# Kernel optimization log

Hardware: AMD Instinct MI355X
Metric: run time of the kernel (lower is better)

## Reference

```python
import jax, jax.numpy as jnp
import numpy as np

B, L, E, H, W = 2, 8192, 1024, 16, 128
HD = E // H  # 64


def setup_inputs() -> dict:
    key = jax.random.key(0)
    ks = jax.random.split(key, 9)
    s = 1.0 / np.sqrt(E)
    inp = {"x": jax.random.normal(ks[0], (B, L, E), jnp.float32)}
    for i, n in enumerate(["Wq", "Wk", "Wv", "Wo"]):
        inp[n] = jax.random.uniform(ks[1 + i], (E, E), jnp.float32, -s, s)
    for i, n in enumerate(["bq", "bk", "bv", "bo"]):
        inp[n] = jax.random.uniform(ks[5 + i], (E,), jnp.float32, -s, s)
    return inp


def _skew_prob(p, w):
    # (..., w, 2w+1) -> (..., w, 3w) with row i right-shifted by i:
    # out[..., i, i+j] = p[..., i, j]  (zeros elsewhere)
    lead = p.shape[:-2]
    M, Lc = p.shape[-2], p.shape[-1]
    p = jnp.pad(p, [(0, 0)] * len(lead) + [(0, 0), (0, M + 1)])
    p = p.reshape(*lead, M * (Lc + M + 1))[..., :-M].reshape(*lead, M, M + Lc)
    return p[..., :-1]


def _sliding_attend(q, k, v, w):
    # q,k,v: (b,h,l,d); banded attention, window w on each side (2w+1 diagonals)
    b, h, l, d = q.shape
    c = l // w
    qc = q.reshape(b, h, c, w, d)
    # per-chunk key/value windows of 3w tokens (w halo each side, zero padded)
    idx = jnp.arange(c)[:, None] * w + jnp.arange(3 * w)[None, :]  # (c, 3w)
    kw = jnp.pad(k, ((0, 0), (0, 0), (w, w), (0, 0)))[:, :, idx]  # (b,h,c,3w,d)
    s = jnp.einsum('bhcqd,bhckd->bhcqk', qc, kw)  # (b,h,c,w,3w)
    # extract band: band[i, j] = s[i, i+j], j in [0, 2w] (offset d = j - w)
    gidx = (jnp.arange(w)[:, None] + jnp.arange(2 * w + 1)[None, :])[None, None, None]
    band = jnp.take_along_axis(s, gidx, axis=-1).reshape(b, h, l, 2 * w + 1)
    # mask out-of-range positions (matches the module's edge -inf loop)
    pos = jnp.arange(l)[:, None] + (jnp.arange(2 * w + 1) - w)[None, :]
    band = jnp.where((pos >= 0) & (pos < l), band, -jnp.inf)
    prob = jax.nn.softmax(band / np.sqrt(d), axis=-1)  # scale by sqrt(head_dim)
    vw = jnp.pad(v, ((0, 0), (0, 0), (w, w), (0, 0)))[:, :, idx]  # (b,h,c,3w,d)
    p3 = _skew_prob(prob.reshape(b, h, c, w, 2 * w + 1), w)  # (b,h,c,w,3w)
    ctx = jnp.einsum('bhcqk,bhckd->bhcqd', p3, vw)
    return ctx.reshape(b, h, l, d)


def reference(x, Wq, Wk, Wv, Wo, bq, bk, bv, bo):
    q = (x @ Wq.T + bq).reshape(B, L, H, HD).transpose(0, 2, 1, 3)
    k = (x @ Wk.T + bk).reshape(B, L, H, HD).transpose(0, 2, 1, 3)
    v = (x @ Wv.T + bv).reshape(B, L, H, HD).transpose(0, 2, 1, 3)
    ctx = _sliding_attend(q, k, v, W)
    ctx = ctx.transpose(0, 2, 1, 3).reshape(B, L, E)
    return ctx @ Wo.T + bo
```

## Files before the change

### kernel.cpp

```cpp
#include <hip/hip_runtime.h>
#include <math.h>

#define B_SZ  2
#define L_SEQ 8192
#define EMB   1024
#define NH    16
#define HDIM  64
#define WIN   128
#define MROWS (B_SZ*L_SEQ)

typedef __attribute__((ext_vector_type(8))) _Float16 f16x8;
typedef __attribute__((ext_vector_type(4))) _Float16 f16x4;
typedef __attribute__((ext_vector_type(4))) float f32x4;

__device__ __forceinline__ void gload16(const void* g, void* l) {
    __builtin_amdgcn_global_load_lds(
        (const __attribute__((address_space(1))) unsigned int*)g,
        (__attribute__((address_space(3))) unsigned int*)l, 16, 0, 0);
}

__global__ __launch_bounds__(256)
void round_all(const float* __restrict__ x,
               const float* __restrict__ wq, const float* __restrict__ wk,
               const float* __restrict__ wv, const float* __restrict__ wo,
               _Float16* __restrict__ xf, _Float16* __restrict__ q16,
               _Float16* __restrict__ k16, _Float16* __restrict__ v16,
               _Float16* __restrict__ o16)
{
    const size_t NX = (size_t)MROWS * EMB, NW = (size_t)EMB * EMB;
    size_t gid = ((size_t)blockIdx.x * 256 + threadIdx.x) * 4;
    const float* src; _Float16* dst; size_t off;
    if (gid < NX)               { src = x;  dst = xf;  off = gid; }
    else if (gid < NX + NW)     { src = wq; dst = q16; off = gid - NX; }
    else if (gid < NX + 2*NW)   { src = wk; dst = k16; off = gid - NX - 2*NW + NW; }
    else if (gid < NX + 3*NW)   { src = wv; dst = v16; off = gid - NX - 2*NW; }
    else                        { src = wo; dst = o16; off = gid - NX - 3*NW; }
    float4 v = *(const float4*)(src + off);
    f16x4 o;
    o[0] = (_Float16)v.x; o[1] = (_Float16)v.y;
    o[2] = (_Float16)v.z; o[3] = (_Float16)v.w;
    *(f16x4*)(dst + off) = o;
}


#define GEMM_CORE(Aptr, Bptr)                                                  \
    const int t = threadIdx.x;                                                 \
    const int wave = t >> 6, lane = t & 63;                                    \
    const int wr = wave >> 2, wc = wave & 3;                                   \
    const int frow = lane & 15, quad = lane >> 4;                              \
    const int srow = t >> 2;                                                   \
    const int schunk = (t & 3) ^ ((t >> 3) & 3);                               \
    size_t gA[2], gB[2];                                                       \
    _Pragma("unroll")                                                          \
    for (int s = 0; s < 2; ++s) {                                              \
        int r = s * 128 + srow;                                                \
        gA[s] = (size_t)(bm + r) * 1024 + schunk * 8;                          \
        gB[s] = (size_t)(bn + r) * 1024 + schunk * 8;                          \
    }                                                                          \
    const int ldst = t * 16;                                                   \
    const int sw = (quad ^ ((frow >> 1) & 3)) * 16;                            \
    int aoff[8], boff[4];                                                      \
    _Pragma("unroll")                                                          \
    for (int i = 0; i < 8; ++i) aoff[i] = (wr * 128 + i * 16 + frow) * 64 + sw;\
    _Pragma("unroll")                                                          \
    for (int j = 0; j < 4; ++j)                                                \
        boff[j] = 32768 + (wc * 64 + j * 16 + frow) * 64 + sw;                 \
    f32x4 acc[8][4] = {};                                                      \
    _Pragma("unroll")                                                          \
    for (int s = 0; s < 2; ++s) {                                              \
        gload16(Aptr + gA[s], smem + s * 8192 + ldst);                         \
        gload16(Bptr + gB[s], smem + 32768 + s * 8192 + ldst);                 \
    }                                                                          \
    for (int kt = 0; kt < 32; ++kt) {                                          \
        const int cur = kt & 1;                                                \
        if (kt < 31) {                                                         \
            const int ko = (kt + 1) * 32;                                      \
            _Pragma("unroll")                                                  \
            for (int s = 0; s < 2; ++s) {                                      \
                gload16(Aptr + gA[s] + ko, smem + (cur ^ 1) * 16384 + s * 8192 + ldst);          \
                gload16(Bptr + gB[s] + ko, smem + 32768 + (cur ^ 1) * 16384 + s * 8192 + ldst);  \
            }                                                                  \
            asm volatile("s_waitcnt vmcnt(4)" ::: "memory");                   \
        } else {                                                               \
            asm volatile("s_waitcnt vmcnt(0)" ::: "memory");                   \
        }                                                                      \
        __builtin_amdgcn_s_barrier();                                          \
        asm volatile("" ::: "memory");                                         \
        const char* Ab = (const char*)smem + cur * 16384;                      \
        f16x8 af[4], bf[4];                                                    \
        _Pragma("unroll")                                                      \
        for (int j = 0; j < 4; ++j) bf[j] = *(const f16x8*)(Ab + boff[j]);     \
        _Pragma("unroll")                                                      \
        for (int i = 0; i < 4; ++i) af[i] = *(const f16x8*)(Ab + aoff[i]);     \
        __builtin_amdgcn_s_setprio(1);                                         \
        _Pragma("unroll")                                                      \
        for (int i = 0; i < 4; ++i)                                            \
            _Pragma("unroll")                                                  \
            for (int j = 0; j < 4; ++j)                                        \
                acc[i][j] = __builtin_amdgcn_mfma_f32_16x16x32_f16(af[i], bf[j], acc[i][j], 0, 0, 0); \
        __builtin_amdgcn_s_setprio(0);                                         \
        _Pragma("unroll")                                                      \
        for (int i = 0; i < 4; ++i) af[i] = *(const f16x8*)(Ab + aoff[i + 4]); \
        __builtin_amdgcn_s_setprio(1);                                         \
        _Pragma("unroll")                                                      \
        for (int i = 0; i < 4; ++i)                                            \
            _Pragma("unroll")                                                  \
            for (int j = 0; j < 4; ++j)                                        \
                acc[i + 4][j] = __builtin_amdgcn_mfma_f32_16x16x32_f16(af[i], bf[j], acc[i + 4][j], 0, 0, 0); \
        __builtin_amdgcn_s_setprio(0);                                         \
        asm volatile("" ::: "memory");                                         \
        __builtin_amdgcn_s_barrier();                                          \
        asm volatile("" ::: "memory");                                         \
    }

__global__ __launch_bounds__(512, 2)
void gemm_qkv(const _Float16* __restrict__ X,
              const _Float16* __restrict__ Wq, const _Float16* __restrict__ Wk,
              const _Float16* __restrict__ Wv,
              const float* __restrict__ bq, const float* __restrict__ bk,
              const float* __restrict__ bv,
              _Float16* __restrict__ qf, _Float16* __restrict__ kf,
              _Float16* __restrict__ vtf)
{
    __shared__ __attribute__((aligned(16))) char smem[65536];

    const int id = blockIdx.x;
    const int row = (id / 96) * 8 + (id & 7);
    const int colq = (id >> 3) % 12;
    const int wsel = colq >> 2;
    const int bm = row * 256, bn = (colq & 3) * 256;
    const _Float16* Bw = wsel == 0 ? Wq : wsel == 1 ? Wk : Wv;
    const float* bias = wsel == 0 ? bq : wsel == 1 ? bk : bv;
    const float scale = wsel == 0 ? 0.125f : 1.0f;

    GEMM_CORE(X, Bw)

    char* Cw = smem + wave * 8192;
    const int bb = bm >> 13;
    const int l0 = (bm & (L_SEQ - 1)) + wr * 128;
    const int h = (bn >> 6) + wc;
    if (wsel < 2) {
        _Float16* dst = wsel == 0 ? qf : kf;
        const size_t hb = ((size_t)(bb * NH + h)) * L_SEQ * HDIM;
        #pragma unroll
        for (int ih = 0; ih < 2; ++ih) {
            asm volatile("" ::: "memory");
            #pragma unroll
            for (int i = 0; i < 4; ++i)
                #pragma unroll
                for (int j = 0; j < 4; ++j) {
                    const int lc = j * 16 + frow;
                    const float bvv = bias[bn + wc * 64 + lc];
                    #pragma unroll
                    for (int r = 0; r < 4; ++r) {
                        const int lr = i * 16 + quad * 4 + r;
                        const int bo = lr * 128 + ((lc * 2) ^ ((lr & 7) << 4));
                        *(_Float16*)(Cw + bo) = (_Float16)((acc[ih * 4 + i][j][r] + bvv) * scale);
                    }
                }
            asm volatile("" ::: "memory");
            #pragma unroll
            for (int p = 0; p < 8; ++p) {
                const int idx = p * 64 + lane;
                const int lr = idx >> 3, seg = idx & 7;
                const int bo = lr * 128 + ((seg * 16) ^ ((lr & 7) << 4));
                uint4 v = *(const uint4*)(Cw + bo);
                *(uint4*)&dst[hb + (size_t)(l0 + ih * 64 + lr) * HDIM + seg * 8] = v;
            }
        }
    } else {
        const size_t hb = ((size_t)(bb * NH + h)) * HDIM * L_SEQ;
        #pragma unroll
        for (int ih = 0; ih < 2; ++ih) {
            asm volatile("" ::: "memory");
            #pragma unroll
            for (int i = 0; i < 4; ++i)
                #pragma unroll
                for (int j = 0; j < 4; ++j) {
                    const int lc = j * 16 + frow;
                    const float bvv = bias[bn + wc * 64 + lc];
                    #pragma unroll
                    for (int r = 0; r < 4; ++r) {
                        const int lr = i * 16 + quad * 4 + r;
                        const int bo = lc * 128 + ((lr * 2) ^ ((lc & 7) << 4));
                        *(_Float16*)(Cw + bo) = (_Float16)(acc[ih * 4 + i][j][r] + bvv);
                    }
                }
            asm volatile("" ::: "memory");
            #pragma unroll
            for (int p = 0; p < 8; ++p) {
                const int idx = p * 64 + lane;
                const int dc = idx >> 3, sl = idx & 7;
                const int bo = dc * 128 + ((sl * 16) ^ ((dc & 7) << 4));
                uint4 v = *(const uint4*)(Cw + bo);
                *(uint4*)&vtf[hb + (size_t)dc * L_SEQ + (l0 + ih * 64 + sl * 8)] = v;
            }
        }
    }
}

__global__ __launch_bounds__(512, 2)
void gemm_out(const _Float16* __restrict__ A, const _Float16* __restrict__ Bwm,
              const float* __restrict__ bias, float* __restrict__ C)
{
    constexpr int N = EMB;
    __shared__ __attribute__((aligned(16))) char smem[65536];

    const int id = blockIdx.x;
    const int row = (id / 32) * 8 + (id & 7);
    const int bm = row * 256, bn = ((id >> 3) & 3) * 256;

    GEMM_CORE(A, Bwm)

    #pragma unroll
    for (int i = 0; i < 8; ++i) {
        int m0 = bm + wr * 128 + i * 16 + quad * 4;
        #pragma unroll
        for (int j = 0; j < 4; ++j) {
            int n = bn + wc * 64 + j * 16 + frow;
            float bvv = bias[n];
            #pragma unroll
            for (int r = 0; r < 4; ++r)
                C[(size_t)(m0 + r) * N + n] = acc[i][j][r] + bvv;
        }
    }
}

__global__ __launch_bounds__(256)
void attn_mfma(const _Float16* __restrict__ qf, const _Float16* __restrict__ kf,
               const _Float16* __restrict__ vtf, _Float16* __restrict__ cf)
{
    __shared__ _Float16 Kf[2][4096], Vf[2][4096];
    __shared__ _Float16 Ps[4][16 * 72];

    const int t = threadIdx.x;
    const int wave = t >> 6, lane = t & 63;
    const int col = lane & 15, quad = lane >> 4;
    const int bh = blockIdx.y;
    const int q0 = blockIdx.x * 128;

    f16x8 qfr[2][2];
    #pragma unroll
    for (int g = 0; g < 2; g++) {
        size_t qidx = ((size_t)bh * L_SEQ + q0 + g * 64 + wave * 16 + col) * HDIM + quad * 8;
        qfr[g][0] = *(const f16x8*)(qf + qidx);
        qfr[g][1] = *(const f16x8*)(qf + qidx + 32);
    }

    f32x4 o[2][4] = {};
    float mrun[2][4], lrun[2][4];
    #pragma unroll
    for (int g = 0; g < 2; g++)
        #pragma unroll
        for (int r = 0; r < 4; r++) { mrun[g][r] = -3e38f; lrun[g][r] = 0.0f; }

    const int srow = t >> 3, sc = t & 7;
    _Float16* Pw = Ps[wave];

    const int ktlo = (q0 == 0) ? 2 : 0;
    const int kthi = (q0 == L_SEQ - 128) ? 4 : 6;

#define STAGE_KV(kt_, bsel_)                                                   \
    {                                                                          \
        const int p0s = q0 - WIN + (kt_) * 64;                                 \
        _Pragma("unroll")                                                      \
        for (int sw2 = 0; sw2 < 2; sw2++) {                                    \
            int rowk = sw2 * 32 + srow;                                        \
            int gq = sc ^ (rowk & 7);                                          \
            size_t kgi = ((size_t)bh * L_SEQ + p0s + rowk) * HDIM + gq * 8;    \
            size_t vgi = ((size_t)bh * HDIM + rowk) * L_SEQ + p0s + gq * 8;    \
            int lb = sw2 * 4096 + wave * 1024;                                 \
            gload16(kf + kgi, (char*)&Kf[bsel_][0] + lb);                      \
            gload16(vtf + vgi, (char*)&Vf[bsel_][0] + lb);                     \
        }                                                                      \
    }

    STAGE_KV(ktlo, 0)

    for (int kt = ktlo; kt < kthi; kt++) {
        const int p0 = q0 - WIN + kt * 64;
        const int cb = (kt - ktlo) & 1;
        if (kt + 1 < kthi) {
            STAGE_KV(kt + 1, cb ^ 1)
            asm volatile("s_waitcnt vmcnt(4)" ::: "memory");
        } else {
            asm volatile("s_waitcnt vmcnt(0)" ::: "memory");
        }
        __builtin_amdgcn_s_barrier();
        asm volatile("" ::: "memory");

        const char* Kb = (const char*)&Kf[cb][0];
        const char* Vb = (const char*)&Vf[cb][0];

        #pragma unroll
        for (int g = 0; g < 2; g++) {
            f32x4 s[4] = {};
            #pragma unroll
            for (int ks = 0; ks < 2; ks++)
                #pragma unroll
                for (int n = 0; n < 4; n++) {
                    int off = (n * 16 + col) * 128 + (((ks * 4 + quad) ^ (col & 7)) * 16);
                    f16x8 kfr = *(const f16x8*)(Kb + off);
                    s[n] = __builtin_amdgcn_mfma_f32_16x16x32_f16(qfr[g][ks], kfr, s[n], 0, 0, 0);
                }
            const int rowb = q0 + g * 64 + wave * 16 + quad * 4;
            #pragma unroll
            for (int n = 0; n < 4; n++)
                #pragma unroll
                for (int r = 0; r < 4; r++) {
                    int dlt = (p0 + n * 16 + col) - (rowb + r);
                    if (dlt < -WIN || dlt > WIN) s[n][r] = -3e38f;
                }
            float mx[4];
            #pragma unroll
            for (int r = 0; r < 4; r++)
                mx[r] = fmaxf(fmaxf(s[0][r], s[1][r]), fmaxf(s[2][r], s[3][r]));
            #pragma unroll
            for (int x = 1; x < 16; x <<= 1)
                #pragma unroll
                for (int r = 0; r < 4; r++)
                    mx[r] = fmaxf(mx[r], __shfl_xor(mx[r], x, 64));
            float alpha[4];
            #pragma unroll
            for (int r = 0; r < 4; r++) {
                float mn = fmaxf(mrun[g][r], mx[r]);
                alpha[r] = __expf(mrun[g][r] - mn);
                mrun[g][r] = mn;
            }
            float sm[4] = {0.f, 0.f, 0.f, 0.f};
            #pragma unroll
            for (int n = 0; n < 4; n++)
                #pragma unroll
                for (int r = 0; r < 4; r++) {
                    float pv = __expf(s[n][r] - mrun[g][r]);
                    sm[r] += pv;
                    Pw[(quad * 4 + r) * 72 + n * 16 + col] = (_Float16)pv;
                }
            #pragma unroll
            for (int x = 1; x < 16; x <<= 1)
                #pragma unroll
                for (int r = 0; r < 4; r++)
                    sm[r] += __shfl_xor(sm[r], x, 64);
            #pragma unroll
            for (int r = 0; r < 4; r++)
                lrun[g][r] = lrun[g][r] * alpha[r] + sm[r];
            #pragma unroll
            for (int n = 0; n < 4; n++)
                #pragma unroll
                for (int r = 0; r < 4; r++)
                    o[g][n][r] *= alpha[r];
            #pragma unroll
            for (int ks = 0; ks < 2; ks++) {
                f16x8 pfr = *(const f16x8*)&Pw[col * 72 + ks * 32 + quad * 8];
                #pragma unroll
                for (int n = 0; n < 4; n++) {
                    int off = (n * 16 + col) * 128 + (((ks * 4 + quad) ^ (col & 7)) * 16);
                    f16x8 vfr = *(const f16x8*)(Vb + off);
                    o[g][n] = __builtin_amdgcn_mfma_f32_16x16x32_f16(pfr, vfr, o[g][n], 0, 0, 0);
                }
            }
        }
        asm volatile("" ::: "memory");
        __builtin_amdgcn_s_barrier();
        asm volatile("" ::: "memory");
    }

    const int b = bh >> 4, h = bh & 15;
    #pragma unroll
    for (int g = 0; g < 2; g++)
        #pragma unroll
        for (int r = 0; r < 4; r++) {
            float inv = 1.0f / lrun[g][r];
            int q = q0 + g * 64 + wave * 16 + quad * 4 + r;
            size_t base = ((size_t)b * L_SEQ + q) * EMB + h * HDIM;
            #pragma unroll
            for (int n = 0; n < 4; n++)
                cf[base + n * 16 + col] = (_Float16)(o[g][n][r] * inv);
        }
}

extern "C" void kernel_launch(void* const* d_in, const int* in_sizes, int n_in,
                              void* d_out, int out_size, void* d_ws, size_t ws_size,
                              hipStream_t stream) {
    const float* x  = (const float*)d_in[0];
    const float* Wq = (const float*)d_in[1];
    const float* Wk = (const float*)d_in[2];
    const float* Wv = (const float*)d_in[3];
    const float* Wo = (const float*)d_in[4];
    const float* bq = (const float*)d_in[5];
    const float* bk = (const float*)d_in[6];
    const float* bv = (const float*)d_in[7];
    const float* bo = (const float*)d_in[8];
    float* out = (float*)d_out;

    const size_t per = (size_t)B_SZ * NH * L_SEQ * HDIM;
    _Float16* w16 = (_Float16*)d_ws;
    _Float16* xf   = w16;
    _Float16* qf   = w16 + per;
    _Float16* kf   = w16 + 2 * per;
    _Float16* vtf  = w16 + 3 * per;
    _Float16* cf   = w16 + 4 * per;
    _Float16* wq16 = w16 + 5 * per;
    _Float16* wk16 = wq16 + 1048576;
    _Float16* wv16 = wq16 + 2 * 1048576;
    _Float16* wo16 = wq16 + 3 * 1048576;

    const int nround = (MROWS * EMB + 4 * EMB * EMB) / 1024;
    round_all<<<nround, dim3(256), 0, stream>>>(x, Wq, Wk, Wv, Wo, xf, wq16, wk16, wv16, wo16);

    gemm_qkv<<<768, dim3(512), 0, stream>>>(xf, wq16, wk16, wv16, bq, bk, bv, qf, kf, vtf);

    attn_mfma<<<dim3(L_SEQ / 128, B_SZ * NH), dim3(256), 0, stream>>>(qf, kf, vtf, cf);

    gemm_out<<<256, dim3(512), 0, stream>>>(cf, wo16, bo, out);
}
```

Measured before the change: 368.4 us.

## Restructure GEMM core into 8-wave ping-pong with K=64 tiles and staged loads

Replaces the K=32 double-buffered GEMM mainloop with a K=64-per-stage loop (16 iterations) that splits each tile into four quadrant MFMA phases, interleaving half-tile global->LDS loads between them with barriers. LDS grows to 128KB per block, which with launch_bounds(512,2) may exceed the per-CU LDS and cut occupancy to one block. The goal is better overlap of memory loads with MFMA and fewer loop iterations, at the cost of many more barriers.

```diff
diff --git a/kernel.cpp b/kernel.cpp
--- a/kernel.cpp
+++ b/kernel.cpp
@@ -43,74 +43,95 @@
 }
 
 
-#define GEMM_CORE(Aptr, Bptr)                                                  \
+#define STAGE_HT(ptr_, tb_, op_, h_, kt_)                                      \
+    {                                                                          \
+        char* d_ = smem + (op_) * 65536 + ((kt_) & 1) * 32768 + (h_) * 16384 + ldst; \
+        const _Float16* s_ = (ptr_) + ((size_t)((tb_) + (h_) * 128 + srow6)) * 1024 + (kt_) * 64 + gch; \
+        gload16(s_, d_);                                                       \
+        gload16(s_ + 64 * 1024, d_ + 8192);                                    \
+    }
+
+#define DSREAD_A(qr_)                                                          \
+    _Pragma("unroll")                                                          \
+    for (int i_ = 0; i_ < 4; ++i_) {                                           \
+        const int ro_ = (qr_) * 8192 + (i_ * 16 + frow) * 128;                 \
+        af[i_][0] = *(const f16x8*)(Ab + ro_ + sb0);                           \
+        af[i_][1] = *(const f16x8*)(Ab + ro_ + sb1);                           \
+    }
+
+#define DSREAD_B(qc_)                                                          \
+    _Pragma("unroll")                                                          \
+    for (int j_ = 0; j_ < 2; ++j_) {                                           \
+        const int ro_ = (brow + (qc_) * 32 + j_ * 16 + frow) * 128;            \
+        bf[j_][0] = *(const f16x8*)(Bb + ro_ + sb0);                           \
+        bf[j_][1] = *(const f16x8*)(Bb + ro_ + sb1);                           \
+    }
+
+#define MFMA16(qr_, qc_)                                                       \
+    __builtin_amdgcn_s_setprio(1);                                             \
+    _Pragma("unroll")                                                          \
+    for (int ks_ = 0; ks_ < 2; ++ks_)                                          \
+        _Pragma("unroll")                                                      \
+        for (int i_ = 0; i_ < 4; ++i_)                                         \
+            _Pragma("unroll")                                                  \
+            for (int j_ = 0; j_ < 2; ++j_)                                     \
+                acc[(qr_) * 4 + i_][(qc_) * 2 + j_] =                          \
+                    __builtin_amdgcn_mfma_f32_16x16x32_f16(                    \
+                        af[i_][ks_], bf[j_][ks_],                              \
+                        acc[(qr_) * 4 + i_][(qc_) * 2 + j_], 0, 0, 0);         \
+    __builtin_amdgcn_s_setprio(0);
+
+#define BARM()                                                                 \
+    asm volatile("" ::: "memory");                                             \
+    __builtin_amdgcn_s_barrier();                                              \
+    asm volatile("" ::: "memory");
+
+#define GEMM8_CORE(Aptr, Bptr)                                                 \
     const int t = threadIdx.x;                                                 \
     const int wave = t >> 6, lane = t & 63;                                    \
     const int wr = wave >> 2, wc = wave & 3;                                   \
     const int frow = lane & 15, quad = lane >> 4;                              \
-    const int srow = t >> 2;                                                   \
-    const int schunk = (t & 3) ^ ((t >> 3) & 3);                               \
-    size_t gA[2], gB[2];                                                       \
-    _Pragma("unroll")                                                          \
-    for (int s = 0; s < 2; ++s) {                                              \
-        int r = s * 128 + srow;                                                \
-        gA[s] = (size_t)(bm + r) * 1024 + schunk * 8;                          \
-        gB[s] = (size_t)(bn + r) * 1024 + schunk * 8;                          \
-    }                                                                          \
+    const int srow6 = t >> 3;                                                  \
+    const int gch = ((t & 7) ^ (srow6 & 7)) * 8;                               \
     const int ldst = t * 16;                                                   \
-    const int sw = (quad ^ ((frow >> 1) & 3)) * 16;                            \
-    int aoff[8], boff[4];                                                      \
-    _Pragma("unroll")                                                          \
-    for (int i = 0; i < 8; ++i) aoff[i] = (wr * 128 + i * 16 + frow) * 64 + sw;\
-    _Pragma("unroll")                                                          \
-    for (int j = 0; j < 4; ++j)                                                \
-        boff[j] = 32768 + (wc * 64 + j * 16 + frow) * 64 + sw;                 \
+    const int sb0 = (quad ^ (frow & 7)) * 16, sb1 = sb0 ^ 64;                  \
+    const int brow = (wc & 1) * 64;                                            \
     f32x4 acc[8][4] = {};                                                      \
-    _Pragma("unroll")                                                          \
-    for (int s = 0; s < 2; ++s) {                                              \
-        gload16(Aptr + gA[s], smem + s * 8192 + ldst);                         \
-        gload16(Bptr + gB[s], smem + 32768 + s * 8192 + ldst);                 \
-    }                                                                          \
-    for (int kt = 0; kt < 32; ++kt) {                                          \
-        const int cur = kt & 1;                                                \
-        if (kt < 31) {                                                         \
-            const int ko = (kt + 1) * 32;                                      \
-            _Pragma("unroll")                                                  \
-            for (int s = 0; s < 2; ++s) {                                      \
-                gload16(Aptr + gA[s] + ko, smem + (cur ^ 1) * 16384 + s * 8192 + ldst);          \
-                gload16(Bptr + gB[s] + ko, smem + 32768 + (cur ^ 1) * 16384 + s * 8192 + ldst);  \
-            }                                                                  \
-            asm volatile("s_waitcnt vmcnt(4)" ::: "memory");                   \
+    f16x8 af[4][2], bf[2][2];                                                  \
+    STAGE_HT(Aptr, bm, 0, 0, 0) STAGE_HT(Aptr, bm, 0, 1, 0)                    \
+    STAGE_HT(Bptr, bn, 1, 0, 0) STAGE_HT(Bptr, bn, 1, 1, 0)                    \
+    for (int kt = 0; kt < 16; ++kt) {                                          \
+        const char* Ab = smem + (kt & 1) * 32768 + wr * 16384;                 \
+        const char* Bb = smem + 65536 + (kt & 1) * 32768 + (wc >> 1) * 16384;  \
+            \
+        if (kt < 15) {                                                         \
+            STAGE_HT(Aptr, bm, 0, 0, kt + 1)                                   \
+            asm volatile("s_waitcnt vmcnt(2)" ::: "memory");                   \
         } else {                                                               \
             asm volatile("s_waitcnt vmcnt(0)" ::: "memory");                   \
         }                                                                      \
-        __builtin_amdgcn_s_barrier();                                          \
-        asm volatile("" ::: "memory");                                         \
-        const char* Ab = (const char*)smem + cur * 16384;                      \
-        f16x8 af[4], bf[4];                                                    \
-        _Pragma("unroll")                                                      \
-        for (int j = 0; j < 4; ++j) bf[j] = *(const f16x8*)(Ab + boff[j]);     \
-        _Pragma("unroll")                                                      \
-        for (int i = 0; i < 4; ++i) af[i] = *(const f16x8*)(Ab + aoff[i]);     \
-        __builtin_amdgcn_s_setprio(1);                                         \
-        _Pragma("unroll")                                                      \
-        for (int i = 0; i < 4; ++i)                                            \
-            _Pragma("unroll")                                                  \
-            for (int j = 0; j < 4; ++j)                                        \
-                acc[i][j] = __builtin_amdgcn_mfma_f32_16x16x32_f16(af[i], bf[j], acc[i][j], 0, 0, 0); \
-        __builtin_amdgcn_s_setprio(0);                                         \
-        _Pragma("unroll")                                                      \
-        for (int i = 0; i < 4; ++i) af[i] = *(const f16x8*)(Ab + aoff[i + 4]); \
-        __builtin_amdgcn_s_setprio(1);                                         \
-        _Pragma("unroll")                                                      \
-        for (int i = 0; i < 4; ++i)                                            \
-            _Pragma("unroll")                                                  \
-            for (int j = 0; j < 4; ++j)                                        \
-                acc[i + 4][j] = __builtin_amdgcn_mfma_f32_16x16x32_f16(af[i], bf[j], acc[i + 4][j], 0, 0, 0); \
-        __builtin_amdgcn_s_setprio(0);                                         \
-        asm volatile("" ::: "memory");                                         \
-        __builtin_amdgcn_s_barrier();                                          \
-        asm volatile("" ::: "memory");                                         \
+        BARM()                                                                 \
+        DSREAD_A(0) DSREAD_B(0)                                                \
+        MFMA16(0, 0)                                                           \
+        BARM()                                                                 \
+                           \
+        DSREAD_B(1)                                                            \
+        if (kt < 15) STAGE_HT(Aptr, bm, 0, 1, kt + 1)                          \
+        BARM()                                                                 \
+        MFMA16(0, 1)                                                           \
+        BARM()                                                                 \
+                           \
+        DSREAD_A(1)                                                            \
+        if (kt < 15) STAGE_HT(Bptr, bn, 1, 0, kt + 1)                          \
+        BARM()                                                                 \
+        MFMA16(1, 1)                                                           \
+        BARM()                                                                 \
+                           \
+        DSREAD_B(0)                                                            \
+        if (kt < 15) STAGE_HT(Bptr, bn, 1, 1, kt + 1)                          \
+        BARM()                                                                 \
+        MFMA16(1, 0)                                                           \
+        BARM()                                                                 \
     }
 
 __global__ __launch_bounds__(512, 2)
@@ -122,7 +143,7 @@
               _Float16* __restrict__ qf, _Float16* __restrict__ kf,
               _Float16* __restrict__ vtf)
 {
-    __shared__ __attribute__((aligned(16))) char smem[65536];
+    __shared__ __attribute__((aligned(16))) char smem[131072];
 
     const int id = blockIdx.x;
     const int row = (id / 96) * 8 + (id & 7);
@@ -133,7 +154,7 @@
     const float* bias = wsel == 0 ? bq : wsel == 1 ? bk : bv;
     const float scale = wsel == 0 ? 0.125f : 1.0f;
 
-    GEMM_CORE(X, Bw)
+    GEMM8_CORE(X, Bw)
 
     char* Cw = smem + wave * 8192;
     const int bb = bm >> 13;
@@ -204,13 +225,13 @@
               const float* __restrict__ bias, float* __restrict__ C)
 {
     constexpr int N = EMB;
-    __shared__ __attribute__((aligned(16))) char smem[65536];
+    __shared__ __attribute__((aligned(16))) char smem[131072];
 
     const int id = blockIdx.x;
     const int row = (id / 32) * 8 + (id & 7);
     const int bm = row * 256, bn = ((id >> 3) & 3) * 256;
 
-    GEMM_CORE(A, Bwm)
+    GEMM8_CORE(A, Bwm)
 
     #pragma unroll
     for (int i = 0; i < 8; ++i) {
```

Result: no change. 370.8 us (+0.6%).
